# Kernel tuning notes

Hardware: AMD Instinct MI355X
Metric: run time of the kernel (lower is better)

The kernel has to match this reference:

```python
import jax, jax.numpy as jnp
import numpy as np
from jax import lax


def _sweep(u, w, V, axis, reverse):
    """One directional min-sum DP sweep (SGM recurrence).

    u: (B, CV, H, W, D) unary costs
    w: (B, 1, H, W)     per-pixel edge weights for this direction
    V: (D, D)           label-context (pairwise smoothness) matrix
    axis: spatial axis of u to scan along (2 = H, 3 = W)
    reverse: scan in decreasing index order
    Returns L: (B, CV, H, W, D) aggregated directional costs,
    L(p, l) = u(p, l) + min_{l'} [ L(p-d, l') + w(p) * V(l', l) ],
    with L = u at the border.
    """
    if reverse:
        u = jnp.flip(u, axis)
        w = jnp.flip(w, axis)
    u_s = jnp.moveaxis(u, axis, 0)   # (T, B, CV, P, D)
    w_s = jnp.moveaxis(w, axis, 0)   # (T, B, 1, P)

    init = u_s[0]

    def step(L_prev, xs):
        u_t, w_t = xs
        # cand[..., l', l] = L_prev[..., l'] + w_t * V[l', l]
        cand = L_prev[..., :, None] + w_t[..., None, None] * V
        L = u_t + jnp.min(cand, axis=-2)
        return L, L

    _, Ls = lax.scan(step, init, (u_s[1:], w_s[1:]))
    L_all = jnp.concatenate([init[None], Ls], axis=0)
    L_all = jnp.moveaxis(L_all, 0, axis)
    if reverse:
        L_all = jnp.flip(L_all, axis)
    return L_all


def setup_inputs() -> dict:
    key = jax.random.key(0)
    k1, k2, k3 = jax.random.split(key, 3)
    B, CV, D, H, W = 4, 1, 21, 512, 512
    N_DIR = 4
    unary = jax.random.uniform(k1, (B, CV, D, H, W), dtype=jnp.float32)
    edge_weights = jax.random.uniform(k2, (B, N_DIR, H, W), dtype=jnp.float32)
    label_context = jax.random.uniform(k3, (D, D), dtype=jnp.float32)
    return {"unary": unary, "edge_weights": edge_weights,
            "label_context": label_context}


def reference(unary, edge_weights, label_context):
    # unary: (B, CV, D, H, W) -> (B, CV, H, W, D) as in MPModule.forward
    u = jnp.transpose(unary, (0, 1, 3, 4, 2))
    # directions: 0 = left->right, 1 = right->left, 2 = top->down, 3 = bottom->up
    dir_cfg = [(3, False), (3, True), (2, False), (2, True)]
    n_dir = len(dir_cfg)
    cost = u
    for d, (axis, reverse) in enumerate(dir_cfg):
        w_d = edge_weights[:, d][:, None]  # (B, 1, H, W)
        L_d = _sweep(u, w_d, label_context, axis, reverse)
        cost = cost + (L_d - u)  # accumulate directional messages
    # permute back to (B, CV, D, H, W) as the module does
    return jnp.transpose(cost, (0, 1, 4, 2, 3))
```

## Files before the change

### kernel.cpp

```cpp
#include <hip/hip_runtime.h>


#define DLBL 21
#define SP 512
#define NB 4
#define SPSP ((long)SP * SP)
#define NELEM ((long)NB * DLBL * SP * SP)

__device__ __forceinline__ void map_task(int i, int& dir, int& line)
{
    if (i < 4096) { dir = i & 1;       line = i >> 1; }
    else          { const int j = i - 4096; dir = 2 + (j & 1); line = j >> 1; }
}

__global__ __launch_bounds__(256)
void transpose2_kernel(const float* __restrict__ u, const float* __restrict__ ew,
                       float* __restrict__ uT, float* l2t, float* l3t)
{
    __shared__ float tile[32][36];
    const int plane = blockIdx.z;
    const float* src;
    float* dst;
    if (plane < NB * DLBL) {
        src = u  + (long)plane * SPSP;
        dst = uT + (long)plane * SPSP;
    } else {
        const int q = plane - NB * DLBL;
        const int b = q >> 1, db = q & 1;
        src = ew + (long)(b * 4 + 2 + db) * SPSP;
        dst = (db ? l3t : l2t) + (long)(b * DLBL + 20) * SPSP;
    }
    const int x0 = blockIdx.x * 32, y0 = blockIdx.y * 32;
    const int r  = threadIdx.x >> 3;
    const int c4 = (threadIdx.x & 7) * 4;
    const float4 v = *(const float4*)&src[(long)(y0 + r) * SP + (x0 + c4)];
    *(float4*)&tile[r][c4] = v;
    __syncthreads();
    float4 ov;
    ov.x = tile[c4 + 0][r];
    ov.y = tile[c4 + 1][r];
    ov.z = tile[c4 + 2][r];
    ov.w = tile[c4 + 3][r];
    *(float4*)&dst[(long)(x0 + r) * SP + (y0 + c4)] = ov;
}

__global__ __launch_bounds__(64, 3)
void sweep6(const float* __restrict__ unary, const float* __restrict__ ew,
            const float* __restrict__ Vmat, const float* __restrict__ uT,
            float* __restrict__ out, float* __restrict__ l1,
            float* l2t, float* l3t)
{
    __shared__ float xch[4][24];
    __shared__ float stage[4][693];
    const int lane = threadIdx.x;
    const int g    = lane / DLBL;
    const int s    = lane - g * DLBL;
    int taskId = blockIdx.x * 3 + (g < 3 ? g : 0);
    if (taskId >= 8192) taskId = 8191;

    int dir, line;
    map_task(taskId, dir, line);
    const int b    = line >> 9;
    const int p    = line & (SP - 1);
    const int axis = dir >> 1;
    const int rev  = dir & 1;
    const float usub = (dir == 0) ? 0.0f : 1.0f;

    float Vc[DLBL];
#pragma unroll
    for (int j = 0; j < DLBL; ++j) Vc[j] = Vmat[j * DLBL + s];

    const float4* ub4 = (const float4*)((axis ? uT : unary)
                        + (long)(b * DLBL + s) * SPSP + (long)p * SP);
    const float* wbase = axis
        ? ((dir == 2 ? l2t : l3t) + (long)(b * DLBL + 20) * SPSP + (long)p * SP)
        : (ew + (long)(b * 4 + dir) * SPSP + (long)p * SP);
    const float4* wb4 = (const float4*)wbase;

    const int frow = lane >> 5, fcol = lane & 31;
    const int stbase = s * 33;

    float* fb[3]; int wrev[3]; bool fvalid[3];
#pragma unroll
    for (int gg = 0; gg < 3; ++gg) {
        const int tid = blockIdx.x * 3 + gg;
        fvalid[gg] = (tid < 8192);
        int d_, ln;
        map_task(fvalid[gg] ? tid : 8191, d_, ln);
        const int bb = ln >> 9;
        const int pp = ln & (SP - 1);
        wrev[gg] = d_ & 1;
        float* dst = (d_ == 0) ? out : (d_ == 1) ? l1 : (d_ == 2) ? l2t : l3t;
        fb[gg] = dst + (long)(bb * DLBL) * SPSP + (long)pp * SP + (long)frow * SPSP;
    }

    float4 uA[4], uB[4], wA[4], wB[4];
    float cur = 0.0f;

#define QIDX(bi, k) (rev ? (127 - 4 * (bi) - (k)) : (4 * (bi) + (k)))

#define LOADBLK(bi, U, W) do {                                              \
    _Pragma("unroll")                                                       \
    for (int k = 0; k < 4; ++k) {                                           \
        const int q_ = QIDX(bi, k);                                         \
        U[k] = ub4[q_]; W[k] = wb4[q_];                                     \
    } } while (0)

#define PROC(bi, U, W, FIRSTB) do {                                         \
    _Pragma("unroll")                                                       \
    for (int k = 0; k < 4; ++k) {                                           \
        const float ua_[4] = {U[k].x, U[k].y, U[k].z, U[k].w};              \
        const float wa_[4] = {W[k].x, W[k].y, W[k].z, W[k].w};              \
        const int q_ = QIDX(bi, k);                                         \
        _Pragma("unroll")                                                   \
        for (int j = 0; j < 4; ++j) {                                       \
            const int   jc  = rev ? 3 - j : j;                              \
            const float u_c = ua_[jc];                                      \
            const float w_c = wa_[jc];                                      \
            const int   t   = q_ * 4 + jc;                                  \
            xch[g][s] = cur;                                                \
            __builtin_amdgcn_wave_barrier();                                \
            float Lp[24];                                                   \
            _Pragma("unroll")                                               \
            for (int qq = 0; qq < 6; ++qq)                                  \
                ((float4*)Lp)[qq] = ((const float4*)(&xch[g][0]))[qq];      \
            __builtin_amdgcn_wave_barrier();                                \
            float c[DLBL];                                                  \
            _Pragma("unroll")                                               \
            for (int jj = 0; jj < DLBL; ++jj)                               \
                c[jj] = fmaf(w_c, Vc[jj], Lp[jj]);                          \
            float m7[7];                                                    \
            _Pragma("unroll")                                               \
            for (int kk = 0; kk < 7; ++kk)                                  \
                m7[kk] = fminf(fminf(c[3*kk], c[3*kk+1]), c[3*kk+2]);       \
            const float ma = fminf(fminf(m7[0], m7[1]), m7[2]);             \
            const float mb = fminf(fminf(m7[3], m7[4]), m7[5]);             \
            const float nv = u_c + fminf(fminf(ma, mb), m7[6]);             \
            cur = ((FIRSTB) && k == 0 && j == 0) ? u_c : nv;                \
            stage[g][stbase + (t & 31)] = fmaf(-usub, u_c, cur);            \
        }                                                                   \
    } } while (0)

#define FLW(w_) do {                                                        \
    __builtin_amdgcn_wave_barrier();                                        \
    _Pragma("unroll")                                                       \
    for (int gg = 0; gg < 3; ++gg) {                                        \
        if (fvalid[gg]) {                                                   \
            float* bp = fb[gg] + (wrev[gg] ? (480 - 32 * (w_))              \
                                           : (32 * (w_)));                  \
            _Pragma("unroll")                                               \
            for (int r2 = 0; r2 < 11; ++r2) {                               \
                const int rr = 2 * r2 + frow;                               \
                if (rr < DLBL) bp[fcol] = stage[gg][rr * 33 + fcol];        \
                bp += 2 * SPSP;                                             \
            }                                                               \
        }                                                                   \
    }                                                                       \
    __builtin_amdgcn_wave_barrier();                                        \
} while (0)

    LOADBLK(0, uA, wA);
    for (int m = 0; m < 16; ++m) {
        LOADBLK(2 * m + 1, uB, wB);
        PROC(2 * m, uA, wA, (m == 0));
        if (m < 15) LOADBLK(2 * m + 2, uA, wA);
        PROC(2 * m + 1, uB, wB, false);
        FLW(m);
    }

#undef QIDX
#undef LOADBLK
#undef PROC
#undef FLW
}

__global__ __launch_bounds__(256)
void finish_kernel(const float* __restrict__ l1, const float* __restrict__ l2t,
                   const float* __restrict__ l3t, float* __restrict__ out)
{
    __shared__ float t2[32][36], t3[32][36];
    const long pb = (long)blockIdx.z * SPSP;
    const int x0 = blockIdx.x * 32, y0 = blockIdx.y * 32;
    const int r  = threadIdx.x >> 3;
    const int c4 = (threadIdx.x & 7) * 4;
    const float4 v2 = *(const float4*)&l2t[pb + (long)(x0 + r) * SP + (y0 + c4)];
    const float4 v3 = *(const float4*)&l3t[pb + (long)(x0 + r) * SP + (y0 + c4)];
    *(float4*)&t2[r][c4] = v2;
    *(float4*)&t3[r][c4] = v3;
    __syncthreads();
    const long o = pb + (long)(y0 + r) * SP + (x0 + c4);
    const float4 a = *(const float4*)&l1[o];
    float4 ov = *(const float4*)&out[o];
    ov.x += a.x + t2[c4 + 0][r] + t3[c4 + 0][r];
    ov.y += a.y + t2[c4 + 1][r] + t3[c4 + 1][r];
    ov.z += a.z + t2[c4 + 2][r] + t3[c4 + 2][r];
    ov.w += a.w + t2[c4 + 3][r] + t3[c4 + 3][r];
    *(float4*)&out[o] = ov;
}

template<int MODE>
__global__ __launch_bounds__(64)
void sweep_fb(const float* __restrict__ unary, const float* __restrict__ ew,
              const float* __restrict__ Vmat, float* __restrict__ out,
              int taskBase)
{
    __shared__ float xch[4][24];
    const int lane = threadIdx.x;
    const int g    = lane / DLBL;
    const int s    = lane - g * DLBL;
    int local = blockIdx.x * 3 + (g < 3 ? g : 0);
    const bool valid = (g < 3) && (local < 2048);
    if (local >= 2048) local = 2047;
    const int taskId = taskBase + local;
    const int dir  = taskId >> 11;
    const int line = taskId & 2047;
    const int b = line >> 9, p = line & (SP - 1);
    const int axis = dir >> 1, rev = dir & 1;

    float Vc[DLBL];
#pragma unroll
    for (int j = 0; j < DLBL; ++j) Vc[j] = Vmat[j * DLBL + s];

    const long ustep = axis ? SP : 1;
    const long ubase = (long)(b * DLBL + s) * SPSP + (axis ? (long)p : (long)p * SP);
    const long wbase = (long)(b * 4 + dir) * SPSP + (axis ? (long)p : (long)p * SP);
    const long uoff  = rev ? -ustep : ustep;
    const long ust   = rev ? (long)(SP - 1) * ustep : 0;

    const float* up = unary + ubase + ust;
    const float* wp = ew    + wbase + ust;
    float*       op = out   + ubase + ust;

    float cur = up[0];
    if (valid && MODE == 1) *op = cur;

    float ub0 = up[uoff], ub1 = up[2*uoff], ub2 = up[3*uoff], ub3 = up[4*uoff];
    float wb0 = wp[uoff], wb1 = wp[2*uoff], wb2 = wp[3*uoff], wb3 = wp[4*uoff];
    float ob0 = 0, ob1 = 0, ob2 = 0, ob3 = 0;
    if (MODE == 2) { ob0 = op[uoff]; ob1 = op[2*uoff]; ob2 = op[3*uoff]; ob3 = op[4*uoff]; }
    const float* upf = up + 4 * uoff;
    const float* wpf = wp + 4 * uoff;
    const float* opf = op + 4 * uoff;

    for (int t = 1; t < SP; ++t) {
        const float u_c = ub0, w_c = wb0, o_c = ob0;
        ub0 = ub1; ub1 = ub2; ub2 = ub3;
        wb0 = wb1; wb1 = wb2; wb2 = wb3;
        if (MODE == 2) { ob0 = ob1; ob1 = ob2; ob2 = ob3; }
        const bool adv = (t + 4) < SP;
        upf += adv ? uoff : 0; wpf += adv ? uoff : 0;
        ub3 = *upf; wb3 = *wpf;
        if (MODE == 2) { opf += adv ? uoff : 0; ob3 = *opf; }

        xch[g][s] = cur;
        __builtin_amdgcn_wave_barrier();
        float Lp[24];
#pragma unroll
        for (int q = 0; q < 6; ++q)
            ((float4*)Lp)[q] = ((const float4*)(&xch[g][0]))[q];
        __builtin_amdgcn_wave_barrier();

        float c[DLBL];
#pragma unroll
        for (int j = 0; j < DLBL; ++j) c[j] = fmaf(w_c, Vc[j], Lp[j]);
        float m7[7];
#pragma unroll
        for (int k = 0; k < 7; ++k)
            m7[k] = fminf(fminf(c[3*k], c[3*k+1]), c[3*k+2]);
        const float ma = fminf(fminf(m7[0], m7[1]), m7[2]);
        const float mb = fminf(fminf(m7[3], m7[4]), m7[5]);
        cur = u_c + fminf(fminf(ma, mb), m7[6]);

        op += uoff;
        if (valid) *op = (MODE == 2) ? (o_c + cur - u_c) : cur;
    }
}

extern "C" void kernel_launch(void* const* d_in, const int* in_sizes, int n_in,
                              void* d_out, int out_size, void* d_ws, size_t ws_size,
                              hipStream_t stream) {
    const float* unary = (const float*)d_in[0];
    const float* ew    = (const float*)d_in[1];
    const float* Vmat  = (const float*)d_in[2];
    float* o = (float*)d_out;

    const size_t needA = (size_t)(4 * NELEM) * sizeof(float);

    if (ws_size >= needA) {
        float* uT  = (float*)d_ws;
        float* l1  = uT + NELEM;
        float* l2t = l1 + NELEM;
        float* l3t = l2t + NELEM;

        dim3 tg(16, 16, NB * DLBL + 8);
        transpose2_kernel<<<tg, 256, 0, stream>>>(unary, ew, uT, l2t, l3t);

        const int grid = (8192 + 2) / 3;
        sweep6<<<grid, 64, 0, stream>>>(unary, ew, Vmat, uT,
                                        o, l1, l2t, l3t);

        finish_kernel<<<dim3(16, 16, NB * DLBL), 256, 0, stream>>>(l1, l2t, l3t, o);
    } else {
        const int grid = (2048 + 2) / 3;
        sweep_fb<1><<<grid, 64, 0, stream>>>(unary, ew, Vmat, o, 0);
        for (int d = 1; d < 4; ++d)
            sweep_fb<2><<<grid, 64, 0, stream>>>(unary, ew, Vmat, o, d * 2048);
    }
}
```

Baseline: 445.7 us.

## Pack five scanlines per wave with two labels per lane in SGM sweep

The sweep kernel now assigns 11 lanes per scanline, with each lane handling two disparity labels, so one 64-lane wave carries five lines instead of three. The aim is to use more of each wave's lanes and raise the useful work per recurrence step. In exchange, each lane does twice the FMA/min work per step, keeps more registers (two 22-entry V columns), and launch bounds drop to 2 waves per SIMD. Blocks are also grouped by direction and line, and the transpose and finish kernels now process four tiles per block to cut block count.

After: 483.7 us. +8.5%, slower.

```diff
diff --git a/kernel.cpp b/kernel.cpp
--- a/kernel.cpp
+++ b/kernel.cpp
@@ -6,15 +6,10 @@
 #define NB 4
 #define SPSP ((long)SP * SP)
 #define NELEM ((long)NB * DLBL * SP * SP)
-
-__device__ __forceinline__ void map_task(int i, int& dir, int& line)
-{
-    if (i < 4096) { dir = i & 1;       line = i >> 1; }
-    else          { const int j = i - 4096; dir = 2 + (j & 1); line = j >> 1; }
-}
+#define BIGF 1e30f
 
 __global__ __launch_bounds__(256)
-void transpose2_kernel(const float* __restrict__ u, const float* __restrict__ ew,
+void transpose3_kernel(const float* __restrict__ u, const float* __restrict__ ew,
                        float* __restrict__ uT, float* l2t, float* l3t)
 {
     __shared__ float tile[32][36];
@@ -30,124 +25,154 @@
         src = ew + (long)(b * 4 + 2 + db) * SPSP;
         dst = (db ? l3t : l2t) + (long)(b * DLBL + 20) * SPSP;
     }
-    const int x0 = blockIdx.x * 32, y0 = blockIdx.y * 32;
+    const int x0 = blockIdx.x * 32;
     const int r  = threadIdx.x >> 3;
     const int c4 = (threadIdx.x & 7) * 4;
-    const float4 v = *(const float4*)&src[(long)(y0 + r) * SP + (x0 + c4)];
-    *(float4*)&tile[r][c4] = v;
-    __syncthreads();
-    float4 ov;
-    ov.x = tile[c4 + 0][r];
-    ov.y = tile[c4 + 1][r];
-    ov.z = tile[c4 + 2][r];
-    ov.w = tile[c4 + 3][r];
-    *(float4*)&dst[(long)(x0 + r) * SP + (y0 + c4)] = ov;
-}
-
-__global__ __launch_bounds__(64, 3)
-void sweep6(const float* __restrict__ unary, const float* __restrict__ ew,
+#pragma unroll
+    for (int it = 0; it < 4; ++it) {
+        const int y0 = (blockIdx.y * 4 + it) * 32;
+        const float4 v = *(const float4*)&src[(long)(y0 + r) * SP + (x0 + c4)];
+        if (it) __syncthreads();
+        *(float4*)&tile[r][c4] = v;
+        __syncthreads();
+        float4 ov;
+        ov.x = tile[c4 + 0][r];
+        ov.y = tile[c4 + 1][r];
+        ov.z = tile[c4 + 2][r];
+        ov.w = tile[c4 + 3][r];
+        *(float4*)&dst[(long)(x0 + r) * SP + (y0 + c4)] = ov;
+    }
+}
+
+__global__ __launch_bounds__(64, 2)
+void sweep7(const float* __restrict__ unary, const float* __restrict__ ew,
             const float* __restrict__ Vmat, const float* __restrict__ uT,
             float* __restrict__ out, float* __restrict__ l1,
             float* l2t, float* l3t)
 {
-    __shared__ float xch[4][24];
-    __shared__ float stage[4][693];
+    __shared__ float xch[5][28];
+    __shared__ float stage[5][693];
     const int lane = threadIdx.x;
-    const int g    = lane / DLBL;
-    const int s    = lane - g * DLBL;
-    int taskId = blockIdx.x * 3 + (g < 3 ? g : 0);
-    if (taskId >= 8192) taskId = 8191;
-
-    int dir, line;
-    map_task(taskId, dir, line);
+    const int gq   = lane / 11;
+    const int gc   = (gq > 4) ? 4 : gq;
+    const int l    = lane - gc * 11;
+    const bool wlane = (lane < 55);
+
+    const int bid   = blockIdx.x;
+    const int axis  = (bid >= 820) ? 1 : 0;
+    const int local = bid - 820 * axis;
+    const int rev   = local & 1;
+    const int lineBase = (local >> 1) * 5;
+    const int dir   = axis * 2 + rev;
+    const float usub = (dir == 0) ? 0.0f : 1.0f;
+
+    const int lg   = lineBase + gc;
+    const int line = (lg > 2047) ? 2047 : lg;
     const int b    = line >> 9;
     const int p    = line & (SP - 1);
-    const int axis = dir >> 1;
-    const int rev  = dir & 1;
-    const float usub = (dir == 0) ? 0.0f : 1.0f;
-
-    float Vc[DLBL];
-#pragma unroll
-    for (int j = 0; j < DLBL; ++j) Vc[j] = Vmat[j * DLBL + s];
-
-    const float4* ub4 = (const float4*)((axis ? uT : unary)
-                        + (long)(b * DLBL + s) * SPSP + (long)p * SP);
-    const float* wbase = axis
+
+    const int d0  = (l > 20) ? 20 : l;
+    const int d1  = l + 11;
+    const int d1c = (d1 > 20) ? 20 : d1;
+
+    float VcA[22], VcB[22];
+#pragma unroll
+    for (int k = 0; k < 22; ++k) {
+        const int lab  = (k & 1) ? ((k >> 1) + 11) : (k >> 1);
+        const bool dum = (lab > 20);
+        const int labc = dum ? 20 : lab;
+        VcA[k] = dum ? 0.0f : Vmat[labc * DLBL + d0];
+        VcB[k] = dum ? 0.0f : Vmat[labc * DLBL + d1c];
+    }
+
+    const float* ubase = axis ? uT : unary;
+    const float4* uA4 = (const float4*)(ubase + (long)(b * DLBL + d0)  * SPSP + (long)p * SP);
+    const float4* uB4 = (const float4*)(ubase + (long)(b * DLBL + d1c) * SPSP + (long)p * SP);
+    const float* wrow = axis
         ? ((dir == 2 ? l2t : l3t) + (long)(b * DLBL + 20) * SPSP + (long)p * SP)
         : (ew + (long)(b * 4 + dir) * SPSP + (long)p * SP);
-    const float4* wb4 = (const float4*)wbase;
+    const float4* w4 = (const float4*)wrow;
 
     const int frow = lane >> 5, fcol = lane & 31;
-    const int stbase = s * 33;
-
-    float* fb[3]; int wrev[3]; bool fvalid[3];
-#pragma unroll
-    for (int gg = 0; gg < 3; ++gg) {
-        const int tid = blockIdx.x * 3 + gg;
-        fvalid[gg] = (tid < 8192);
-        int d_, ln;
-        map_task(fvalid[gg] ? tid : 8191, d_, ln);
-        const int bb = ln >> 9;
-        const int pp = ln & (SP - 1);
-        wrev[gg] = d_ & 1;
-        float* dst = (d_ == 0) ? out : (d_ == 1) ? l1 : (d_ == 2) ? l2t : l3t;
-        fb[gg] = dst + (long)(bb * DLBL) * SPSP + (long)pp * SP + (long)frow * SPSP;
-    }
-
-    float4 uA[4], uB[4], wA[4], wB[4];
-    float cur = 0.0f;
+
+    float* fb[5]; bool fvalid[5];
+    float* dst = (dir == 0) ? out : (dir == 1) ? l1 : (dir == 2) ? l2t : l3t;
+#pragma unroll
+    for (int gg = 0; gg < 5; ++gg) {
+        const int lgg = lineBase + gg;
+        fvalid[gg] = (lgg < 2048);
+        const int lc = fvalid[gg] ? lgg : 2047;
+        fb[gg] = dst + (long)((lc >> 9) * DLBL) * SPSP + (long)(lc & (SP - 1)) * SP
+                     + (long)frow * SPSP;
+    }
+
+    float4 AU[4], AV[4], AW[4], BU[4], BV[4], BW[4];
+    float curA = 0.0f, curB = 0.0f;
 
 #define QIDX(bi, k) (rev ? (127 - 4 * (bi) - (k)) : (4 * (bi) + (k)))
 
-#define LOADBLK(bi, U, W) do {                                              \
+#define LOADBLK(bi, U, V2, W) do {                                          \
     _Pragma("unroll")                                                       \
     for (int k = 0; k < 4; ++k) {                                           \
         const int q_ = QIDX(bi, k);                                         \
-        U[k] = ub4[q_]; W[k] = wb4[q_];                                     \
+        U[k] = uA4[q_]; V2[k] = uB4[q_]; W[k] = w4[q_];                     \
     } } while (0)
 
-#define PROC(bi, U, W, FIRSTB) do {                                         \
+#define PROC(bi, U, V2, W, FIRSTB) do {                                     \
     _Pragma("unroll")                                                       \
     for (int k = 0; k < 4; ++k) {                                           \
-        const float ua_[4] = {U[k].x, U[k].y, U[k].z, U[k].w};              \
-        const float wa_[4] = {W[k].x, W[k].y, W[k].z, W[k].w};              \
+        const float uaA[4] = {U[k].x,  U[k].y,  U[k].z,  U[k].w};           \
+        const float uaB[4] = {V2[k].x, V2[k].y, V2[k].z, V2[k].w};          \
+        const float wa[4]  = {W[k].x,  W[k].y,  W[k].z,  W[k].w};           \
         const int q_ = QIDX(bi, k);                                         \
         _Pragma("unroll")                                                   \
         for (int j = 0; j < 4; ++j) {                                       \
             const int   jc  = rev ? 3 - j : j;                              \
-            const float u_c = ua_[jc];                                      \
-            const float w_c = wa_[jc];                                      \
+            const float uAc = uaA[jc], uBc = uaB[jc], wc = wa[jc];          \
             const int   t   = q_ * 4 + jc;                                  \
-            xch[g][s] = cur;                                                \
+            if (wlane) *(float2*)&xch[gc][2 * l] = make_float2(curA, curB); \
             __builtin_amdgcn_wave_barrier();                                \
             float Lp[24];                                                   \
             _Pragma("unroll")                                               \
             for (int qq = 0; qq < 6; ++qq)                                  \
-                ((float4*)Lp)[qq] = ((const float4*)(&xch[g][0]))[qq];      \
+                ((float4*)Lp)[qq] = ((const float4*)(&xch[gc][0]))[qq];     \
             __builtin_amdgcn_wave_barrier();                                \
-            float c[DLBL];                                                  \
+            float cA_[22], cB_[22];                                         \
             _Pragma("unroll")                                               \
-            for (int jj = 0; jj < DLBL; ++jj)                               \
-                c[jj] = fmaf(w_c, Vc[jj], Lp[jj]);                          \
-            float m7[7];                                                    \
+            for (int kk = 0; kk < 22; ++kk) {                               \
+                cA_[kk] = fmaf(wc, VcA[kk], Lp[kk]);                        \
+                cB_[kk] = fmaf(wc, VcB[kk], Lp[kk]);                        \
+            }                                                               \
+            float mA[11], mB[11];                                           \
             _Pragma("unroll")                                               \
-            for (int kk = 0; kk < 7; ++kk)                                  \
-                m7[kk] = fminf(fminf(c[3*kk], c[3*kk+1]), c[3*kk+2]);       \
-            const float ma = fminf(fminf(m7[0], m7[1]), m7[2]);             \
-            const float mb = fminf(fminf(m7[3], m7[4]), m7[5]);             \
-            const float nv = u_c + fminf(fminf(ma, mb), m7[6]);             \
-            cur = ((FIRSTB) && k == 0 && j == 0) ? u_c : nv;                \
-            stage[g][stbase + (t & 31)] = fmaf(-usub, u_c, cur);            \
+            for (int kk = 0; kk < 11; ++kk) {                               \
+                mA[kk] = fminf(cA_[2*kk], cA_[2*kk+1]);                     \
+                mB[kk] = fminf(cB_[2*kk], cB_[2*kk+1]);                     \
+            }                                                               \
+            const float rA = fminf(fminf(fminf(fminf(mA[0],mA[1]),          \
+                fminf(mA[2],mA[3])), fminf(fminf(mA[4],mA[5]),              \
+                fminf(mA[6],mA[7]))), fminf(fminf(mA[8],mA[9]), mA[10]));   \
+            const float rB = fminf(fminf(fminf(fminf(mB[0],mB[1]),          \
+                fminf(mB[2],mB[3])), fminf(fminf(mB[4],mB[5]),              \
+                fminf(mB[6],mB[7]))), fminf(fminf(mB[8],mB[9]), mB[10]));   \
+            float nvA = uAc + rA, nvB = uBc + rB;                           \
+            if ((FIRSTB) && k == 0 && j == 0) { nvA = uAc; nvB = uBc; }     \
+            curA = nvA;                                                     \
+            curB = (l == 10) ? BIGF : nvB;    \
+            const int col = t & 31;                                         \
+            if (wlane) stage[gc][l * 33 + col] = fmaf(-usub, uAc, curA);    \
+            if (wlane && l < 10)                                            \
+                stage[gc][(l + 11) * 33 + col] = fmaf(-usub, uBc, curB);    \
         }                                                                   \
     } } while (0)
 
 #define FLW(w_) do {                                                        \
     __builtin_amdgcn_wave_barrier();                                        \
+    const int w0 = rev ? (480 - 32 * (w_)) : (32 * (w_));                   \
     _Pragma("unroll")                                                       \
-    for (int gg = 0; gg < 3; ++gg) {                                        \
+    for (int gg = 0; gg < 5; ++gg) {                                        \
         if (fvalid[gg]) {                                                   \
-            float* bp = fb[gg] + (wrev[gg] ? (480 - 32 * (w_))              \
-                                           : (32 * (w_)));                  \
+            float* bp = fb[gg] + w0;                                        \
             _Pragma("unroll")                                               \
             for (int r2 = 0; r2 < 11; ++r2) {                               \
                 const int rr = 2 * r2 + frow;                               \
@@ -159,12 +184,12 @@
     __builtin_amdgcn_wave_barrier();                                        \
 } while (0)
 
-    LOADBLK(0, uA, wA);
+    LOADBLK(0, AU, AV, AW);
     for (int m = 0; m < 16; ++m) {
-        LOADBLK(2 * m + 1, uB, wB);
-        PROC(2 * m, uA, wA, (m == 0));
-        if (m < 15) LOADBLK(2 * m + 2, uA, wA);
-        PROC(2 * m + 1, uB, wB, false);
+        LOADBLK(2 * m + 1, BU, BV, BW);
+        PROC(2 * m, AU, AV, AW, (m == 0));
+        if (m < 15) LOADBLK(2 * m + 2, AU, AV, AW);
+        PROC(2 * m + 1, BU, BV, BW, false);
         FLW(m);
     }
 
@@ -175,27 +200,32 @@
 }
 
 __global__ __launch_bounds__(256)
-void finish_kernel(const float* __restrict__ l1, const float* __restrict__ l2t,
-                   const float* __restrict__ l3t, float* __restrict__ out)
+void finish2_kernel(const float* __restrict__ l1, const float* __restrict__ l2t,
+                    const float* __restrict__ l3t, float* __restrict__ out)
 {
     __shared__ float t2[32][36], t3[32][36];
     const long pb = (long)blockIdx.z * SPSP;
-    const int x0 = blockIdx.x * 32, y0 = blockIdx.y * 32;
+    const int x0 = blockIdx.x * 32;
     const int r  = threadIdx.x >> 3;
     const int c4 = (threadIdx.x & 7) * 4;
-    const float4 v2 = *(const float4*)&l2t[pb + (long)(x0 + r) * SP + (y0 + c4)];
-    const float4 v3 = *(const float4*)&l3t[pb + (long)(x0 + r) * SP + (y0 + c4)];
-    *(float4*)&t2[r][c4] = v2;
-    *(float4*)&t3[r][c4] = v3;
-    __syncthreads();
-    const long o = pb + (long)(y0 + r) * SP + (x0 + c4);
-    const float4 a = *(const float4*)&l1[o];
-    float4 ov = *(const float4*)&out[o];
-    ov.x += a.x + t2[c4 + 0][r] + t3[c4 + 0][r];
-    ov.y += a.y + t2[c4 + 1][r] + t3[c4 + 1][r];
-    ov.z += a.z + t2[c4 + 2][r] + t3[c4 + 2][r];
-    ov.w += a.w + t2[c4 + 3][r] + t3[c4 + 3][r];
-    *(float4*)&out[o] = ov;
+#pragma unroll
+    for (int it = 0; it < 4; ++it) {
+        const int y0 = (blockIdx.y * 4 + it) * 32;
+        const float4 v2 = *(const float4*)&l2t[pb + (long)(x0 + r) * SP + (y0 + c4)];
+        const float4 v3 = *(const float4*)&l3t[pb + (long)(x0 + r) * SP + (y0 + c4)];
+        if (it) __syncthreads();
+        *(float4*)&t2[r][c4] = v2;
+        *(float4*)&t3[r][c4] = v3;
+        __syncthreads();
+        const long o = pb + (long)(y0 + r) * SP + (x0 + c4);
+        const float4 a = *(const float4*)&l1[o];
+        float4 ov = *(const float4*)&out[o];
+        ov.x += a.x + t2[c4 + 0][r] + t3[c4 + 0][r];
+        ov.y += a.y + t2[c4 + 1][r] + t3[c4 + 1][r];
+        ov.z += a.z + t2[c4 + 2][r] + t3[c4 + 2][r];
+        ov.w += a.w + t2[c4 + 3][r] + t3[c4 + 3][r];
+        *(float4*)&out[o] = ov;
+    }
 }
 
 template<int MODE>
@@ -292,14 +322,13 @@
         float* l2t = l1 + NELEM;
         float* l3t = l2t + NELEM;
 
-        dim3 tg(16, 16, NB * DLBL + 8);
-        transpose2_kernel<<<tg, 256, 0, stream>>>(unary, ew, uT, l2t, l3t);
-
-        const int grid = (8192 + 2) / 3;
-        sweep6<<<grid, 64, 0, stream>>>(unary, ew, Vmat, uT,
+        transpose3_kernel<<<dim3(16, 4, NB * DLBL + 8), 256, 0, stream>>>(
+            unary, ew, uT, l2t, l3t);
+
+        sweep7<<<1640, 64, 0, stream>>>(unary, ew, Vmat, uT,
                                         o, l1, l2t, l3t);
 
-        finish_kernel<<<dim3(16, 16, NB * DLBL), 256, 0, stream>>>(l1, l2t, l3t, o);
+        finish2_kernel<<<dim3(16, 4, NB * DLBL), 256, 0, stream>>>(l1, l2t, l3t, o);
     } else {
         const int grid = (2048 + 2) / 3;
         sweep_fb<1><<<grid, 64, 0, stream>>>(unary, ew, Vmat, o, 0);
```
